# Optimization experiments

Measured on AMD Instinct MI355X. Metric: run time of the kernel, lower is better.

## Reference

```python
import jax, jax.numpy as jnp
import numpy as np
from jax import lax

T = 1.0      # terminal time
SIGMA = 1.0  # diffusion coefficient
N, D, P, M, H = 16384, 16, 8, 50, 128


def setup_inputs() -> dict:
    key = jax.random.key(0)
    ks = jax.random.split(key, 8)
    scale1 = 1.0 / np.sqrt(1 + D + P)
    scale2 = 1.0 / np.sqrt(H)
    return {
        "initial_states": jax.random.normal(ks[0], (N, D), jnp.float32),
        "initial_values": jax.random.normal(ks[1], (N,), jnp.float32),
        "observations": jax.random.normal(ks[2], (N, P), jnp.float32),
        "noise": jax.random.normal(ks[3], (M, N, D), jnp.float32),
        "W1": jax.random.normal(ks[4], (1 + D + P, H), jnp.float32) * scale1,
        "b1": jnp.zeros((H,), jnp.float32),
        "W2": jax.random.normal(ks[5], (H, H), jnp.float32) * scale2,
        "b2": jnp.zeros((H,), jnp.float32),
        "W3": jax.random.normal(ks[6], (H, D), jnp.float32) * scale2,
        "b3": jnp.zeros((D,), jnp.float32),
    }


def reference(initial_states, initial_values, observations, noise,
              W1, b1, W2, b2, W3, b3):
    """Euler-Maruyama rollout of simulate_SDEs: joint (X, V) SDE with
    per-step Z-network drift. drift b(X) = -X (OU process)."""
    m_steps = noise.shape[0]
    dt = jnp.asarray(T / m_steps, initial_states.dtype)
    sqrt_dt = jnp.sqrt(dt)
    times = jnp.arange(m_steps, dtype=initial_states.dtype) * dt  # time[m]

    def z_net(t, X, Y):
        tcol = jnp.full((X.shape[0], 1), t, X.dtype)
        h = jnp.concatenate([tcol, X, Y], axis=1)      # (N, 1+d+p)
        h = jax.nn.relu(h @ W1 + b1)
        h = jax.nn.relu(h @ W2 + b2)
        return h @ W3 + b3                             # (N, d)

    def step(carry, inp):
        X, V = carry
        eps, t = inp
        Wn = sqrt_dt * eps                             # Brownian increment
        Z = z_net(t, X, observations)
        drift_V = 0.5 * jnp.sum(Z * Z, axis=1)
        V = V + dt * drift_V + jnp.sum(Z * Wn, axis=1)
        X = X + dt * (-X) + SIGMA * Wn                 # b(X) = -X
        return (X, V), None

    (X, V), _ = lax.scan(step, (initial_states, initial_values), (noise, times))
    return X, V
```

## Files before the change

kernel.cpp:

```cpp
#include <hip/hip_runtime.h>

typedef __bf16   bf16x8 __attribute__((ext_vector_type(8)));
typedef float    f32x4  __attribute__((ext_vector_type(4)));
typedef float    f32x2  __attribute__((ext_vector_type(2)));
typedef uint32_t u32x4  __attribute__((ext_vector_type(4)));

constexpr int N_ = 16384;
constexpr int D_ = 16;
constexpr int P_ = 8;
constexpr int H_ = 128;
constexpr int M_ = 50;

__device__ __forceinline__ uint32_t pk_bf16(float a, float b) {
    uint32_t ua = __builtin_bit_cast(uint32_t, a) + 0x8000u;
    uint32_t ub = __builtin_bit_cast(uint32_t, b) + 0x8000u;
    return __builtin_amdgcn_perm(ub, ua, 0x07060302u);
}
__device__ __forceinline__ uint32_t cvtpk(float a, float b) {
    uint32_t r;
    asm("v_cvt_pk_bf16_f32 %0, %1, %2" : "=v"(r) : "v"(a), "v"(b));
    return r;
}
__device__ __forceinline__ uint32_t cvtpk_relu(float a, float b) {
    return cvtpk(fmaxf(a, 0.0f), fmaxf(b, 0.0f));
}

__device__ __forceinline__ bf16x8 lds_ldv(const bf16x8* p) {
    u32x4 v = *(volatile const u32x4*)p;
    return __builtin_bit_cast(bf16x8, v);
}

__global__ __launch_bounds__(128, 2)
void sde_fused(const float* __restrict__ X0,
               const float* __restrict__ V0,
               const float* __restrict__ Yobs,
               const float* __restrict__ noise,
               const float* __restrict__ W1, const float* __restrict__ b1,
               const float* __restrict__ W2, const float* __restrict__ b2,
               const float* __restrict__ W3, const float* __restrict__ b3,
               float* __restrict__ out)
{
    const int tid  = threadIdx.x;
    const int lane = tid & 63;
    const int half = tid >> 6;
    const int n    = lane & 15;
    const int q    = lane >> 4;
    const int gr   = blockIdx.x * 16 + n;

    const float dt   = 0.02f;
    const float sqdt = 0.1414213562373095f;

    __shared__ bf16x8 w2lds[8][4][64];
    __shared__ float  vpart[16];

#pragma unroll
    for (int cc = 0; cc < 4; ++cc) {
        const int ct = half * 4 + cc;
#pragma unroll
        for (int kt = 0; kt < 4; ++kt) {
            u32x4 u;
#pragma unroll
            for (int w = 0; w < 4; ++w) {
                int h0 = (kt * 2 + (w >> 1)) * 16 + q * 4 + (w & 1) * 2;
                u[w] = pk_bf16(W2[h0 * H_ + ct * 16 + n],
                               W2[(h0 + 1) * H_ + ct * 16 + n]);
            }
            w2lds[ct][kt][lane] = __builtin_bit_cast(bf16x8, u);
        }
    }

    bf16x8 w1f[8];
#pragma unroll
    for (int ct = 0; ct < 8; ++ct) {
        u32x4 u;
        u[0] = pk_bf16(W1[(1 + q * 4 + 0) * H_ + ct * 16 + n],
                       W1[(1 + q * 4 + 1) * H_ + ct * 16 + n]);
        u[1] = pk_bf16(W1[(1 + q * 4 + 2) * H_ + ct * 16 + n],
                       W1[(1 + q * 4 + 3) * H_ + ct * 16 + n]);
        u[2] = pk_bf16(W1[(17 + q * 2 + 0) * H_ + ct * 16 + n],
                       W1[(17 + q * 2 + 1) * H_ + ct * 16 + n]);
        u[3] = (q == 0) ? pk_bf16(b1[ct * 16 + n], W1[ct * 16 + n]) : 0u;
        w1f[ct] = __builtin_bit_cast(bf16x8, u);
    }
    bf16x8 w3f[4];
#pragma unroll
    for (int kt = 0; kt < 4; ++kt) {
        u32x4 u;
#pragma unroll
        for (int w = 0; w < 4; ++w) {
            int h0 = (kt * 2 + (w >> 1)) * 16 + q * 4 + (w & 1) * 2;
            u[w] = pk_bf16(W3[h0 * D_ + n], W3[(h0 + 1) * D_ + n]);
        }
        w3f[kt] = __builtin_bit_cast(bf16x8, u);
    }
    f32x4 b2r[8];
#pragma unroll
    for (int ct = 0; ct < 8; ++ct)
#pragma unroll
        for (int r = 0; r < 4; ++r) b2r[ct][r] = b2[ct * 16 + q * 4 + r];
    f32x4 b3r;
#pragma unroll
    for (int r = 0; r < 4; ++r) b3r[r] = b3[q * 4 + r];

    __syncthreads();

    f32x4 x = *(const f32x4*)&X0[gr * D_ + q * 4];
    f32x2 y2 = *(const f32x2*)&Yobs[gr * P_ + q * 2];
    const uint32_t yw = pk_bf16(y2[0], y2[1]);
    const float* npb = noise + (size_t)gr * D_ + q * 4;

    if (half == 1) {
#pragma unroll 2
        for (int m = 0; m < 25; ++m) {
            f32x4 e = *(const f32x4*)(npb + (size_t)m * N_ * D_);
#pragma unroll
            for (int r = 0; r < 4; ++r)
                x[r] = fmaf(x[r], 0.98f, sqdt * e[r]);
        }
    }

    const int s0 = half * 25;
    float t = half ? 0.5f : 0.0f;
    f32x4 e0 = *(const f32x4*)(npb + (size_t)s0 * N_ * D_);
    float vacc = 0.0f;

#pragma unroll 1
    for (int i = 0; i < 25; ++i) {
        const int m  = s0 + i;
        const int mn = (m + 1 < M_) ? (m + 1) : (M_ - 1);
        f32x4 e1 = *(const f32x4*)(npb + (size_t)mn * N_ * D_);

        u32x4 au;
        au[0] = cvtpk(x[0], x[1]);
        au[1] = cvtpk(x[2], x[3]);
        au[2] = yw;
        au[3] = (q == 0) ? cvtpk(1.0f, t) : 0u;
        bf16x8 a0 = __builtin_bit_cast(bf16x8, au);

        f32x4 h1c[8];
#pragma unroll
        for (int ct = 0; ct < 8; ++ct)
            h1c[ct] = __builtin_amdgcn_mfma_f32_16x16x32_bf16(
                w1f[ct], a0, (f32x4){0.f, 0.f, 0.f, 0.f}, 0, 0, 0);

        bf16x8 h1b[4];
#pragma unroll
        for (int kt = 0; kt < 4; ++kt) {
            u32x4 u;
            u[0] = cvtpk_relu(h1c[2 * kt][0], h1c[2 * kt][1]);
            u[1] = cvtpk_relu(h1c[2 * kt][2], h1c[2 * kt][3]);
            u[2] = cvtpk_relu(h1c[2 * kt + 1][0], h1c[2 * kt + 1][1]);
            u[3] = cvtpk_relu(h1c[2 * kt + 1][2], h1c[2 * kt + 1][3]);
            h1b[kt] = __builtin_bit_cast(bf16x8, u);
        }

        bf16x8 w2buf[2][4];
#pragma unroll
        for (int kt = 0; kt < 4; ++kt) w2buf[0][kt] = lds_ldv(&w2lds[0][kt][lane]);

        f32x4 hprev;
        bf16x8 h2b[4];
#pragma unroll
        for (int ct = 0; ct < 8; ++ct) {
            if (ct < 7) {
#pragma unroll
                for (int kt = 0; kt < 4; ++kt)
                    w2buf[(ct + 1) & 1][kt] = lds_ldv(&w2lds[ct + 1][kt][lane]);
            }
            f32x4 c = b2r[ct];
#pragma unroll
            for (int kt = 0; kt < 4; ++kt)
                c = __builtin_amdgcn_mfma_f32_16x16x32_bf16(
                    w2buf[ct & 1][kt], h1b[kt], c, 0, 0, 0);
            if ((ct & 1) == 0) {
                hprev = c;
            } else {
                u32x4 u;
                u[0] = cvtpk_relu(hprev[0], hprev[1]);
                u[1] = cvtpk_relu(hprev[2], hprev[3]);
                u[2] = cvtpk_relu(c[0], c[1]);
                u[3] = cvtpk_relu(c[2], c[3]);
                h2b[ct >> 1] = __builtin_bit_cast(bf16x8, u);
            }
        }

        f32x4 za = __builtin_amdgcn_mfma_f32_16x16x32_bf16(w3f[0], h2b[0], b3r, 0, 0, 0);
        za = __builtin_amdgcn_mfma_f32_16x16x32_bf16(w3f[1], h2b[1], za, 0, 0, 0);
        f32x4 zb = __builtin_amdgcn_mfma_f32_16x16x32_bf16(
            w3f[2], h2b[2], (f32x4){0.f, 0.f, 0.f, 0.f}, 0, 0, 0);
        zb = __builtin_amdgcn_mfma_f32_16x16x32_bf16(w3f[3], h2b[3], zb, 0, 0, 0);

#pragma unroll
        for (int r = 0; r < 4; ++r) {
            float z  = za[r] + zb[r];
            float wn = sqdt * e0[r];
            vacc = fmaf(z, wn, fmaf(0.01f * z, z, vacc));
            x[r] = fmaf(x[r], 0.98f, wn);
        }

        e0 = e1;
        t += dt;
    }

    float part = vacc;
    part += __shfl_xor(part, 16);
    part += __shfl_xor(part, 32);

    if (half == 0 && q == 0) vpart[n] = part;
    __syncthreads();
    if (half == 1) {
        *(f32x4*)&out[gr * D_ + q * 4] = x;
        if (q == 0) out[N_ * D_ + gr] = V0[gr] + vpart[n] + part;
    }
}

extern "C" void kernel_launch(void* const* d_in, const int* in_sizes, int n_in,
                              void* d_out, int out_size, void* d_ws, size_t ws_size,
                              hipStream_t stream)
{
    const float* X0 = (const float*)d_in[0];
    const float* V0 = (const float*)d_in[1];
    const float* Y  = (const float*)d_in[2];
    const float* nz = (const float*)d_in[3];
    const float* W1 = (const float*)d_in[4];
    const float* b1 = (const float*)d_in[5];
    const float* W2 = (const float*)d_in[6];
    const float* b2 = (const float*)d_in[7];
    const float* W3 = (const float*)d_in[8];
    const float* b3 = (const float*)d_in[9];
    float* out = (float*)d_out;

    sde_fused<<<N_ / 16, 128, 0, stream>>>(X0, V0, Y, nz, W1, b1, W2, b2, W3, b3, out);
}
```

Baseline: 158.7 us.

## Keep W2 in registers and stream W1, W3 and b2 from LDS

Swaps which weights live where. W2 fragments (32 bf16x8) are now held in VGPRs instead of being reloaded from LDS every step. The smaller W1, W3 and b2 operands move to a shared LDS buffer and are software-prefetched around the MFMA chains. The layer-1 MFMAs and ReLU packing are also interleaved with the W1 prefetches. This aims to cut per-step LDS traffic and latency on the largest GEMM, at the cost of higher register pressure under launch_bounds(128,2) and extra LDS loads for the smaller matrices.

```diff
diff --git a/kernel.cpp b/kernel.cpp
--- a/kernel.cpp
+++ b/kernel.cpp
@@ -25,9 +25,13 @@
     return cvtpk(fmaxf(a, 0.0f), fmaxf(b, 0.0f));
 }
 
-__device__ __forceinline__ bf16x8 lds_ldv(const bf16x8* p) {
+__device__ __forceinline__ bf16x8 lds_ldv8(const void* p) {
     u32x4 v = *(volatile const u32x4*)p;
     return __builtin_bit_cast(bf16x8, v);
+}
+__device__ __forceinline__ f32x4 lds_ldvf(const void* p) {
+    u32x4 v = *(volatile const u32x4*)p;
+    return __builtin_bit_cast(f32x4, v);
 }
 
 __global__ __launch_bounds__(128, 2)
@@ -50,12 +54,39 @@
     const float dt   = 0.02f;
     const float sqdt = 0.1414213562373095f;
 
-    __shared__ bf16x8 w2lds[8][4][64];
-    __shared__ float  vpart[16];
-
-#pragma unroll
-    for (int cc = 0; cc < 4; ++cc) {
-        const int ct = half * 4 + cc;
+    __shared__ __align__(16) unsigned char smem[12864];
+
+    if (half == 0) {
+#pragma unroll
+        for (int ct = 0; ct < 8; ++ct) {
+            u32x4 u;
+            u[0] = pk_bf16(W1[(1 + q * 4 + 0) * H_ + ct * 16 + n],
+                           W1[(1 + q * 4 + 1) * H_ + ct * 16 + n]);
+            u[1] = pk_bf16(W1[(1 + q * 4 + 2) * H_ + ct * 16 + n],
+                           W1[(1 + q * 4 + 3) * H_ + ct * 16 + n]);
+            u[2] = pk_bf16(W1[(17 + q * 2 + 0) * H_ + ct * 16 + n],
+                           W1[(17 + q * 2 + 1) * H_ + ct * 16 + n]);
+            u[3] = (q == 0) ? pk_bf16(b1[ct * 16 + n], W1[ct * 16 + n]) : 0u;
+            *(u32x4*)(smem + ct * 1024 + lane * 16) = u;
+            __builtin_amdgcn_sched_barrier(0);
+        }
+#pragma unroll
+        for (int kt = 0; kt < 4; ++kt) {
+            u32x4 u;
+#pragma unroll
+            for (int w = 0; w < 4; ++w) {
+                int h0 = (kt * 2 + (w >> 1)) * 16 + q * 4 + (w & 1) * 2;
+                u[w] = pk_bf16(W3[h0 * D_ + n], W3[(h0 + 1) * D_ + n]);
+            }
+            *(u32x4*)(smem + 8192 + kt * 1024 + lane * 16) = u;
+            __builtin_amdgcn_sched_barrier(0);
+        }
+        if (lane < 32) *(f32x4*)(smem + 12288 + lane * 16) = *(const f32x4*)&b2[lane * 4];
+    }
+
+    bf16x8 w2f[8][4];
+#pragma unroll
+    for (int ct = 0; ct < 8; ++ct) {
 #pragma unroll
         for (int kt = 0; kt < 4; ++kt) {
             u32x4 u;
@@ -65,42 +96,12 @@
                 u[w] = pk_bf16(W2[h0 * H_ + ct * 16 + n],
                                W2[(h0 + 1) * H_ + ct * 16 + n]);
             }
-            w2lds[ct][kt][lane] = __builtin_bit_cast(bf16x8, u);
-        }
-    }
-
-    bf16x8 w1f[8];
-#pragma unroll
-    for (int ct = 0; ct < 8; ++ct) {
-        u32x4 u;
-        u[0] = pk_bf16(W1[(1 + q * 4 + 0) * H_ + ct * 16 + n],
-                       W1[(1 + q * 4 + 1) * H_ + ct * 16 + n]);
-        u[1] = pk_bf16(W1[(1 + q * 4 + 2) * H_ + ct * 16 + n],
-                       W1[(1 + q * 4 + 3) * H_ + ct * 16 + n]);
-        u[2] = pk_bf16(W1[(17 + q * 2 + 0) * H_ + ct * 16 + n],
-                       W1[(17 + q * 2 + 1) * H_ + ct * 16 + n]);
-        u[3] = (q == 0) ? pk_bf16(b1[ct * 16 + n], W1[ct * 16 + n]) : 0u;
-        w1f[ct] = __builtin_bit_cast(bf16x8, u);
-    }
-    bf16x8 w3f[4];
-#pragma unroll
-    for (int kt = 0; kt < 4; ++kt) {
-        u32x4 u;
-#pragma unroll
-        for (int w = 0; w < 4; ++w) {
-            int h0 = (kt * 2 + (w >> 1)) * 16 + q * 4 + (w & 1) * 2;
-            u[w] = pk_bf16(W3[h0 * D_ + n], W3[(h0 + 1) * D_ + n]);
-        }
-        w3f[kt] = __builtin_bit_cast(bf16x8, u);
-    }
-    f32x4 b2r[8];
-#pragma unroll
-    for (int ct = 0; ct < 8; ++ct)
-#pragma unroll
-        for (int r = 0; r < 4; ++r) b2r[ct][r] = b2[ct * 16 + q * 4 + r];
-    f32x4 b3r;
-#pragma unroll
-    for (int r = 0; r < 4; ++r) b3r[r] = b3[q * 4 + r];
+            w2f[ct][kt] = __builtin_bit_cast(bf16x8, u);
+        }
+        __builtin_amdgcn_sched_barrier(0);
+    }
+
+    f32x4 b3r = *(const f32x4*)&b3[q * 4];
 
     __syncthreads();
 
@@ -123,6 +124,19 @@
     float t = half ? 0.5f : 0.0f;
     f32x4 e0 = *(const f32x4*)(npb + (size_t)s0 * N_ * D_);
     float vacc = 0.0f;
+
+    const uint32_t lofs = (uint32_t)lane * 16u;
+    const uint32_t qofs = (uint32_t)q * 16u;
+
+    bf16x8 w1buf[4];
+#pragma unroll
+    for (int k = 0; k < 4; ++k) w1buf[k] = lds_ldv8(smem + k * 1024 + lofs);
+    bf16x8 w3buf[2];
+    w3buf[0] = lds_ldv8(smem + 8192 + 0 * 1024 + lofs);
+    w3buf[1] = lds_ldv8(smem + 8192 + 1 * 1024 + lofs);
+    f32x4 b2buf[2];
+    b2buf[0] = lds_ldvf(smem + 12288 + 0 * 64 + qofs);
+    b2buf[1] = lds_ldvf(smem + 12288 + 1 * 64 + qofs);
 
 #pragma unroll 1
     for (int i = 0; i < 25; ++i) {
@@ -137,58 +151,58 @@
         au[3] = (q == 0) ? cvtpk(1.0f, t) : 0u;
         bf16x8 a0 = __builtin_bit_cast(bf16x8, au);
 
-        f32x4 h1c[8];
-#pragma unroll
-        for (int ct = 0; ct < 8; ++ct)
-            h1c[ct] = __builtin_amdgcn_mfma_f32_16x16x32_bf16(
-                w1f[ct], a0, (f32x4){0.f, 0.f, 0.f, 0.f}, 0, 0, 0);
-
         bf16x8 h1b[4];
-#pragma unroll
-        for (int kt = 0; kt < 4; ++kt) {
-            u32x4 u;
-            u[0] = cvtpk_relu(h1c[2 * kt][0], h1c[2 * kt][1]);
-            u[1] = cvtpk_relu(h1c[2 * kt][2], h1c[2 * kt][3]);
-            u[2] = cvtpk_relu(h1c[2 * kt + 1][0], h1c[2 * kt + 1][1]);
-            u[3] = cvtpk_relu(h1c[2 * kt + 1][2], h1c[2 * kt + 1][3]);
-            h1b[kt] = __builtin_bit_cast(bf16x8, u);
-        }
-
-        bf16x8 w2buf[2][4];
-#pragma unroll
-        for (int kt = 0; kt < 4; ++kt) w2buf[0][kt] = lds_ldv(&w2lds[0][kt][lane]);
-
-        f32x4 hprev;
-        bf16x8 h2b[4];
+        f32x4 hodd;
 #pragma unroll
         for (int ct = 0; ct < 8; ++ct) {
-            if (ct < 7) {
-#pragma unroll
-                for (int kt = 0; kt < 4; ++kt)
-                    w2buf[(ct + 1) & 1][kt] = lds_ldv(&w2lds[ct + 1][kt][lane]);
-            }
-            f32x4 c = b2r[ct];
-#pragma unroll
-            for (int kt = 0; kt < 4; ++kt)
-                c = __builtin_amdgcn_mfma_f32_16x16x32_bf16(
-                    w2buf[ct & 1][kt], h1b[kt], c, 0, 0, 0);
+            const int b = ct & 3;
+            f32x4 h = __builtin_amdgcn_mfma_f32_16x16x32_bf16(
+                w1buf[b], a0, (f32x4){0.f, 0.f, 0.f, 0.f}, 0, 0, 0);
+            w1buf[b] = lds_ldv8(smem + ((ct + 4) & 7) * 1024 + lofs);
             if ((ct & 1) == 0) {
-                hprev = c;
+                hodd = h;
             } else {
                 u32x4 u;
-                u[0] = cvtpk_relu(hprev[0], hprev[1]);
-                u[1] = cvtpk_relu(hprev[2], hprev[3]);
-                u[2] = cvtpk_relu(c[0], c[1]);
-                u[3] = cvtpk_relu(c[2], c[3]);
-                h2b[ct >> 1] = __builtin_bit_cast(bf16x8, u);
+                u[0] = cvtpk_relu(hodd[0], hodd[1]);
+                u[1] = cvtpk_relu(hodd[2], hodd[3]);
+                u[2] = cvtpk_relu(h[0], h[1]);
+                u[3] = cvtpk_relu(h[2], h[3]);
+                h1b[ct >> 1] = __builtin_bit_cast(bf16x8, u);
             }
         }
 
-        f32x4 za = __builtin_amdgcn_mfma_f32_16x16x32_bf16(w3f[0], h2b[0], b3r, 0, 0, 0);
-        za = __builtin_amdgcn_mfma_f32_16x16x32_bf16(w3f[1], h2b[1], za, 0, 0, 0);
+        bf16x8 h2b[4];
+#pragma unroll
+        for (int ctp = 0; ctp < 4; ++ctp) {
+            f32x4 c0 = b2buf[0];
+            f32x4 c1 = b2buf[1];
+            b2buf[0] = lds_ldvf(smem + 12288 + ((2 * ctp + 2) & 7) * 64 + qofs);
+            b2buf[1] = lds_ldvf(smem + 12288 + ((2 * ctp + 3) & 7) * 64 + qofs);
+#pragma unroll
+            for (int kt = 0; kt < 4; ++kt)
+                c0 = __builtin_amdgcn_mfma_f32_16x16x32_bf16(
+                    w2f[2 * ctp][kt], h1b[kt], c0, 0, 0, 0);
+#pragma unroll
+            for (int kt = 0; kt < 4; ++kt)
+                c1 = __builtin_amdgcn_mfma_f32_16x16x32_bf16(
+                    w2f[2 * ctp + 1][kt], h1b[kt], c1, 0, 0, 0);
+            u32x4 u;
+            u[0] = cvtpk_relu(c0[0], c0[1]);
+            u[1] = cvtpk_relu(c0[2], c0[3]);
+            u[2] = cvtpk_relu(c1[0], c1[1]);
+            u[3] = cvtpk_relu(c1[2], c1[3]);
+            h2b[ctp] = __builtin_bit_cast(bf16x8, u);
+        }
+
+        f32x4 za = __builtin_amdgcn_mfma_f32_16x16x32_bf16(w3buf[0], h2b[0], b3r, 0, 0, 0);
+        w3buf[0] = lds_ldv8(smem + 8192 + 2 * 1024 + lofs);
+        za = __builtin_amdgcn_mfma_f32_16x16x32_bf16(w3buf[1], h2b[1], za, 0, 0, 0);
+        w3buf[1] = lds_ldv8(smem + 8192 + 3 * 1024 + lofs);
         f32x4 zb = __builtin_amdgcn_mfma_f32_16x16x32_bf16(
-            w3f[2], h2b[2], (f32x4){0.f, 0.f, 0.f, 0.f}, 0, 0, 0);
-        zb = __builtin_amdgcn_mfma_f32_16x16x32_bf16(w3f[3], h2b[3], zb, 0, 0, 0);
+            w3buf[0], h2b[2], (f32x4){0.f, 0.f, 0.f, 0.f}, 0, 0, 0);
+        w3buf[0] = lds_ldv8(smem + 8192 + 0 * 1024 + lofs);
+        zb = __builtin_amdgcn_mfma_f32_16x16x32_bf16(w3buf[1], h2b[3], zb, 0, 0, 0);
+        w3buf[1] = lds_ldv8(smem + 8192 + 1 * 1024 + lofs);
 
 #pragma unroll
         for (int r = 0; r < 4; ++r) {
@@ -206,11 +220,12 @@
     part += __shfl_xor(part, 16);
     part += __shfl_xor(part, 32);
 
-    if (half == 0 && q == 0) vpart[n] = part;
+    if (half == 0 && q == 0) *(float*)(smem + 12800 + n * 4) = part;
     __syncthreads();
     if (half == 1) {
         *(f32x4*)&out[gr * D_ + q * 4] = x;
-        if (q == 0) out[N_ * D_ + gr] = V0[gr] + vpart[n] + part;
+        if (q == 0)
+            out[N_ * D_ + gr] = V0[gr] + *(const float*)(smem + 12800 + n * 4) + part;
     }
 }
 
```

Result: slower. 172.3 us (+8.5%).

## Switch MLP to 32x32x16 MFMA with register-resident W2, 32 rows per block

Applied to the files above, without the earlier changes.

Replaces the 16x16x32 MFMA tiling with 32x32x16 MFMAs, so each block handles 32 samples instead of 16. All of W2 is now held in registers (4x8 bf16x8 fragments per lane) instead of being staged through LDS and reloaded every step, and the b2 bias is injected through an extra rank-1 MFMA. The goal is to cut LDS traffic and per-sample instruction overhead. In exchange register pressure rises sharply, so launch bounds drop to one block per SIMD-equivalent, the grid halves to 512 blocks and occupancy falls, which may leave latency exposed. The W3 MFMA also wastes half its output rows because D is 16.

```diff
diff --git a/kernel.cpp b/kernel.cpp
--- a/kernel.cpp
+++ b/kernel.cpp
@@ -2,7 +2,7 @@
 
 typedef __bf16   bf16x8 __attribute__((ext_vector_type(8)));
 typedef float    f32x4  __attribute__((ext_vector_type(4)));
-typedef float    f32x2  __attribute__((ext_vector_type(2)));
+typedef float    f32x16 __attribute__((ext_vector_type(16)));
 typedef uint32_t u32x4  __attribute__((ext_vector_type(4)));
 
 constexpr int N_ = 16384;
@@ -25,12 +25,7 @@
     return cvtpk(fmaxf(a, 0.0f), fmaxf(b, 0.0f));
 }
 
-__device__ __forceinline__ bf16x8 lds_ldv(const bf16x8* p) {
-    u32x4 v = *(volatile const u32x4*)p;
-    return __builtin_bit_cast(bf16x8, v);
-}
-
-__global__ __launch_bounds__(128, 2)
+__global__ __launch_bounds__(128, 1)
 void sde_fused(const float* __restrict__ X0,
                const float* __restrict__ V0,
                const float* __restrict__ Yobs,
@@ -43,174 +38,214 @@
     const int tid  = threadIdx.x;
     const int lane = tid & 63;
     const int half = tid >> 6;
-    const int n    = lane & 15;
-    const int q    = lane >> 4;
-    const int gr   = blockIdx.x * 16 + n;
+    const int n    = lane & 31;
+    const int hi   = lane >> 5;
+    const int gr   = blockIdx.x * 32 + n;
 
     const float dt   = 0.02f;
     const float sqdt = 0.1414213562373095f;
 
-    __shared__ bf16x8 w2lds[8][4][64];
-    __shared__ float  vpart[16];
-
-#pragma unroll
-    for (int cc = 0; cc < 4; ++cc) {
-        const int ct = half * 4 + cc;
-#pragma unroll
-        for (int kt = 0; kt < 4; ++kt) {
+    const f32x16 Z16 = {0.f,0.f,0.f,0.f,0.f,0.f,0.f,0.f,
+                        0.f,0.f,0.f,0.f,0.f,0.f,0.f,0.f};
+
+    bf16x8 a1f[4][2];
+#pragma unroll
+    for (int mt = 0; mt < 4; ++mt) {
+        const int col = mt * 32 + n;
+        u32x4 u;
+        u[0] = pk_bf16(W1[(1 + 4*hi) * H_ + col],  W1[(2 + 4*hi) * H_ + col]);
+        u[1] = pk_bf16(W1[(3 + 4*hi) * H_ + col],  W1[(4 + 4*hi) * H_ + col]);
+        u[2] = pk_bf16(W1[(9 + 4*hi) * H_ + col],  W1[(10 + 4*hi) * H_ + col]);
+        u[3] = pk_bf16(W1[(11 + 4*hi) * H_ + col], W1[(12 + 4*hi) * H_ + col]);
+        a1f[mt][0] = __builtin_bit_cast(bf16x8, u);
+        u32x4 v;
+        v[0] = hi ? pk_bf16(W1[0 * H_ + col], b1[col])
+                  : pk_bf16(W1[17 * H_ + col], W1[18 * H_ + col]);
+        v[1] = hi ? 0u : pk_bf16(W1[19 * H_ + col], W1[20 * H_ + col]);
+        v[2] = hi ? 0u : pk_bf16(W1[21 * H_ + col], W1[22 * H_ + col]);
+        v[3] = hi ? 0u : pk_bf16(W1[23 * H_ + col], W1[24 * H_ + col]);
+        a1f[mt][1] = __builtin_bit_cast(bf16x8, v);
+    }
+
+    bf16x8 a2f[4][8], a2b[4];
+#pragma unroll
+    for (int mt = 0; mt < 4; ++mt) {
+        const int col = mt * 32 + n;
+#pragma unroll
+        for (int kt = 0; kt < 8; ++kt) {
+            const int r0 = kt * 16 + 4 * hi;
             u32x4 u;
-#pragma unroll
-            for (int w = 0; w < 4; ++w) {
-                int h0 = (kt * 2 + (w >> 1)) * 16 + q * 4 + (w & 1) * 2;
-                u[w] = pk_bf16(W2[h0 * H_ + ct * 16 + n],
-                               W2[(h0 + 1) * H_ + ct * 16 + n]);
-            }
-            w2lds[ct][kt][lane] = __builtin_bit_cast(bf16x8, u);
-        }
-    }
-
-    bf16x8 w1f[8];
-#pragma unroll
-    for (int ct = 0; ct < 8; ++ct) {
+            u[0] = pk_bf16(W2[(r0 + 0) * H_ + col],  W2[(r0 + 1) * H_ + col]);
+            u[1] = pk_bf16(W2[(r0 + 2) * H_ + col],  W2[(r0 + 3) * H_ + col]);
+            u[2] = pk_bf16(W2[(r0 + 8) * H_ + col],  W2[(r0 + 9) * H_ + col]);
+            u[3] = pk_bf16(W2[(r0 + 10) * H_ + col], W2[(r0 + 11) * H_ + col]);
+            a2f[mt][kt] = __builtin_bit_cast(bf16x8, u);
+        }
+        u32x4 ub;
+        ub[0] = hi ? 0u : pk_bf16(b2[col], 0.0f);
+        ub[1] = 0u; ub[2] = 0u; ub[3] = 0u;
+        a2b[mt] = __builtin_bit_cast(bf16x8, ub);
+    }
+
+    bf16x8 a3f[8];
+    const bool mv = (n < 16);
+#pragma unroll
+    for (int kt = 0; kt < 8; ++kt) {
+        const int r0 = kt * 16 + 4 * hi;
+        float f0 = mv ? W3[(r0 + 0) * D_ + n] : 0.0f;
+        float f1 = mv ? W3[(r0 + 1) * D_ + n] : 0.0f;
+        float f2 = mv ? W3[(r0 + 2) * D_ + n] : 0.0f;
+        float f3 = mv ? W3[(r0 + 3) * D_ + n] : 0.0f;
+        float f4 = mv ? W3[(r0 + 8) * D_ + n] : 0.0f;
+        float f5 = mv ? W3[(r0 + 9) * D_ + n] : 0.0f;
+        float f6 = mv ? W3[(r0 + 10) * D_ + n] : 0.0f;
+        float f7 = mv ? W3[(r0 + 11) * D_ + n] : 0.0f;
         u32x4 u;
-        u[0] = pk_bf16(W1[(1 + q * 4 + 0) * H_ + ct * 16 + n],
-                       W1[(1 + q * 4 + 1) * H_ + ct * 16 + n]);
-        u[1] = pk_bf16(W1[(1 + q * 4 + 2) * H_ + ct * 16 + n],
-                       W1[(1 + q * 4 + 3) * H_ + ct * 16 + n]);
-        u[2] = pk_bf16(W1[(17 + q * 2 + 0) * H_ + ct * 16 + n],
-                       W1[(17 + q * 2 + 1) * H_ + ct * 16 + n]);
-        u[3] = (q == 0) ? pk_bf16(b1[ct * 16 + n], W1[ct * 16 + n]) : 0u;
-        w1f[ct] = __builtin_bit_cast(bf16x8, u);
-    }
-    bf16x8 w3f[4];
-#pragma unroll
-    for (int kt = 0; kt < 4; ++kt) {
-        u32x4 u;
-#pragma unroll
-        for (int w = 0; w < 4; ++w) {
-            int h0 = (kt * 2 + (w >> 1)) * 16 + q * 4 + (w & 1) * 2;
-            u[w] = pk_bf16(W3[h0 * D_ + n], W3[(h0 + 1) * D_ + n]);
-        }
-        w3f[kt] = __builtin_bit_cast(bf16x8, u);
-    }
-    f32x4 b2r[8];
-#pragma unroll
-    for (int ct = 0; ct < 8; ++ct)
-#pragma unroll
-        for (int r = 0; r < 4; ++r) b2r[ct][r] = b2[ct * 16 + q * 4 + r];
-    f32x4 b3r;
-#pragma unroll
-    for (int r = 0; r < 4; ++r) b3r[r] = b3[q * 4 + r];
-
-    __syncthreads();
-
-    f32x4 x = *(const f32x4*)&X0[gr * D_ + q * 4];
-    f32x2 y2 = *(const f32x2*)&Yobs[gr * P_ + q * 2];
-    const uint32_t yw = pk_bf16(y2[0], y2[1]);
-    const float* npb = noise + (size_t)gr * D_ + q * 4;
+        u[0] = pk_bf16(f0, f1);
+        u[1] = pk_bf16(f2, f3);
+        u[2] = pk_bf16(f4, f5);
+        u[3] = pk_bf16(f6, f7);
+        a3f[kt] = __builtin_bit_cast(bf16x8, u);
+    }
+
+    f32x16 b3c = Z16;
+#pragma unroll
+    for (int r = 0; r < 8; ++r) b3c[r] = b3[(r & 3) + 8 * (r >> 2) + 4 * hi];
+
+    u32x4 fbu;
+    fbu[0] = hi ? 0u : pk_bf16(1.0f, 0.0f);
+    fbu[1] = 0u; fbu[2] = 0u; fbu[3] = 0u;
+    const bf16x8 fbias = __builtin_bit_cast(bf16x8, fbu);
+
+    f32x4 y0 = *(const f32x4*)&Yobs[gr * P_];
+    f32x4 y1 = *(const f32x4*)&Yobs[gr * P_ + 4];
+    const uint32_t yw0 = pk_bf16(y0[0], y0[1]);
+    const uint32_t yw1 = pk_bf16(y0[2], y0[3]);
+    const uint32_t yw2 = pk_bf16(y1[0], y1[1]);
+    const uint32_t yw3 = pk_bf16(y1[2], y1[3]);
+
+    f32x4 xA = *(const f32x4*)&X0[gr * D_ + 4 * hi];
+    f32x4 xB = *(const f32x4*)&X0[gr * D_ + 8 + 4 * hi];
+    const float* npb = noise + (size_t)gr * D_ + 4 * hi;
 
     if (half == 1) {
 #pragma unroll 2
         for (int m = 0; m < 25; ++m) {
-            f32x4 e = *(const f32x4*)(npb + (size_t)m * N_ * D_);
-#pragma unroll
-            for (int r = 0; r < 4; ++r)
-                x[r] = fmaf(x[r], 0.98f, sqdt * e[r]);
+            f32x4 eA = *(const f32x4*)(npb + (size_t)m * N_ * D_);
+            f32x4 eB = *(const f32x4*)(npb + (size_t)m * N_ * D_ + 8);
+#pragma unroll
+            for (int r = 0; r < 4; ++r) {
+                xA[r] = fmaf(xA[r], 0.98f, sqdt * eA[r]);
+                xB[r] = fmaf(xB[r], 0.98f, sqdt * eB[r]);
+            }
         }
     }
 
     const int s0 = half * 25;
     float t = half ? 0.5f : 0.0f;
-    f32x4 e0 = *(const f32x4*)(npb + (size_t)s0 * N_ * D_);
+    f32x4 eA0 = *(const f32x4*)(npb + (size_t)s0 * N_ * D_);
+    f32x4 eB0 = *(const f32x4*)(npb + (size_t)s0 * N_ * D_ + 8);
     float vacc = 0.0f;
 
 #pragma unroll 1
     for (int i = 0; i < 25; ++i) {
         const int m  = s0 + i;
         const int mn = (m + 1 < M_) ? (m + 1) : (M_ - 1);
-        f32x4 e1 = *(const f32x4*)(npb + (size_t)mn * N_ * D_);
-
-        u32x4 au;
-        au[0] = cvtpk(x[0], x[1]);
-        au[1] = cvtpk(x[2], x[3]);
-        au[2] = yw;
-        au[3] = (q == 0) ? cvtpk(1.0f, t) : 0u;
-        bf16x8 a0 = __builtin_bit_cast(bf16x8, au);
-
-        f32x4 h1c[8];
-#pragma unroll
-        for (int ct = 0; ct < 8; ++ct)
-            h1c[ct] = __builtin_amdgcn_mfma_f32_16x16x32_bf16(
-                w1f[ct], a0, (f32x4){0.f, 0.f, 0.f, 0.f}, 0, 0, 0);
-
-        bf16x8 h1b[4];
-#pragma unroll
-        for (int kt = 0; kt < 4; ++kt) {
+        f32x4 eA1 = *(const f32x4*)(npb + (size_t)mn * N_ * D_);
+        f32x4 eB1 = *(const f32x4*)(npb + (size_t)mn * N_ * D_ + 8);
+
+        u32x4 g0u;
+        g0u[0] = cvtpk(xA[0], xA[1]);
+        g0u[1] = cvtpk(xA[2], xA[3]);
+        g0u[2] = cvtpk(xB[0], xB[1]);
+        g0u[3] = cvtpk(xB[2], xB[3]);
+        bf16x8 g0 = __builtin_bit_cast(bf16x8, g0u);
+        u32x4 g1u;
+        g1u[0] = hi ? cvtpk(t, 1.0f) : yw0;
+        g1u[1] = hi ? 0u : yw1;
+        g1u[2] = hi ? 0u : yw2;
+        g1u[3] = hi ? 0u : yw3;
+        bf16x8 g1 = __builtin_bit_cast(bf16x8, g1u);
+
+        f32x16 acc1[4];
+#pragma unroll
+        for (int mt = 0; mt < 4; ++mt) {
+            f32x16 c = __builtin_amdgcn_mfma_f32_32x32x16_bf16(a1f[mt][0], g0, Z16, 0, 0, 0);
+            acc1[mt]  = __builtin_amdgcn_mfma_f32_32x32x16_bf16(a1f[mt][1], g1, c, 0, 0, 0);
+        }
+
+        bf16x8 hb[8];
+#pragma unroll
+        for (int kt = 0; kt < 8; ++kt) {
+            const int r0 = 8 * (kt & 1);
+            const f32x16 A = acc1[kt >> 1];
             u32x4 u;
-            u[0] = cvtpk_relu(h1c[2 * kt][0], h1c[2 * kt][1]);
-            u[1] = cvtpk_relu(h1c[2 * kt][2], h1c[2 * kt][3]);
-            u[2] = cvtpk_relu(h1c[2 * kt + 1][0], h1c[2 * kt + 1][1]);
-            u[3] = cvtpk_relu(h1c[2 * kt + 1][2], h1c[2 * kt + 1][3]);
-            h1b[kt] = __builtin_bit_cast(bf16x8, u);
-        }
-
-        bf16x8 w2buf[2][4];
-#pragma unroll
-        for (int kt = 0; kt < 4; ++kt) w2buf[0][kt] = lds_ldv(&w2lds[0][kt][lane]);
-
-        f32x4 hprev;
-        bf16x8 h2b[4];
-#pragma unroll
-        for (int ct = 0; ct < 8; ++ct) {
-            if (ct < 7) {
-#pragma unroll
-                for (int kt = 0; kt < 4; ++kt)
-                    w2buf[(ct + 1) & 1][kt] = lds_ldv(&w2lds[ct + 1][kt][lane]);
-            }
-            f32x4 c = b2r[ct];
-#pragma unroll
-            for (int kt = 0; kt < 4; ++kt)
-                c = __builtin_amdgcn_mfma_f32_16x16x32_bf16(
-                    w2buf[ct & 1][kt], h1b[kt], c, 0, 0, 0);
-            if ((ct & 1) == 0) {
-                hprev = c;
-            } else {
-                u32x4 u;
-                u[0] = cvtpk_relu(hprev[0], hprev[1]);
-                u[1] = cvtpk_relu(hprev[2], hprev[3]);
-                u[2] = cvtpk_relu(c[0], c[1]);
-                u[3] = cvtpk_relu(c[2], c[3]);
-                h2b[ct >> 1] = __builtin_bit_cast(bf16x8, u);
-            }
-        }
-
-        f32x4 za = __builtin_amdgcn_mfma_f32_16x16x32_bf16(w3f[0], h2b[0], b3r, 0, 0, 0);
-        za = __builtin_amdgcn_mfma_f32_16x16x32_bf16(w3f[1], h2b[1], za, 0, 0, 0);
-        f32x4 zb = __builtin_amdgcn_mfma_f32_16x16x32_bf16(
-            w3f[2], h2b[2], (f32x4){0.f, 0.f, 0.f, 0.f}, 0, 0, 0);
-        zb = __builtin_amdgcn_mfma_f32_16x16x32_bf16(w3f[3], h2b[3], zb, 0, 0, 0);
+            u[0] = cvtpk_relu(A[r0 + 0], A[r0 + 1]);
+            u[1] = cvtpk_relu(A[r0 + 2], A[r0 + 3]);
+            u[2] = cvtpk_relu(A[r0 + 4], A[r0 + 5]);
+            u[3] = cvtpk_relu(A[r0 + 6], A[r0 + 7]);
+            hb[kt] = __builtin_bit_cast(bf16x8, u);
+        }
+
+        f32x16 acc2[4];
+#pragma unroll
+        for (int mt = 0; mt < 4; ++mt) {
+            f32x16 c = __builtin_amdgcn_mfma_f32_32x32x16_bf16(a2b[mt], fbias, Z16, 0, 0, 0);
+#pragma unroll
+            for (int kt = 0; kt < 8; ++kt)
+                c = __builtin_amdgcn_mfma_f32_32x32x16_bf16(a2f[mt][kt], hb[kt], c, 0, 0, 0);
+            acc2[mt] = c;
+        }
+
+        bf16x8 gb[8];
+#pragma unroll
+        for (int kt = 0; kt < 8; ++kt) {
+            const int r0 = 8 * (kt & 1);
+            const f32x16 A = acc2[kt >> 1];
+            u32x4 u;
+            u[0] = cvtpk_relu(A[r0 + 0], A[r0 + 1]);
+            u[1] = cvtpk_relu(A[r0 + 2], A[r0 + 3]);
+            u[2] = cvtpk_relu(A[r0 + 4], A[r0 + 5]);
+            u[3] = cvtpk_relu(A[r0 + 6], A[r0 + 7]);
+            gb[kt] = __builtin_bit_cast(bf16x8, u);
+        }
+
+        f32x16 acc3 = b3c;
+#pragma unroll
+        for (int kt = 0; kt < 8; ++kt)
+            acc3 = __builtin_amdgcn_mfma_f32_32x32x16_bf16(a3f[kt], gb[kt], acc3, 0, 0, 0);
 
 #pragma unroll
         for (int r = 0; r < 4; ++r) {
-            float z  = za[r] + zb[r];
-            float wn = sqdt * e0[r];
+            float z  = acc3[r];
+            float wn = sqdt * eA0[r];
             vacc = fmaf(z, wn, fmaf(0.01f * z, z, vacc));
-            x[r] = fmaf(x[r], 0.98f, wn);
-        }
-
-        e0 = e1;
+        }
+#pragma unroll
+        for (int r = 0; r < 4; ++r) {
+            float z  = acc3[4 + r];
+            float wn = sqdt * eB0[r];
+            vacc = fmaf(z, wn, fmaf(0.01f * z, z, vacc));
+        }
+#pragma unroll
+        for (int r = 0; r < 4; ++r) {
+            xA[r] = fmaf(xA[r], 0.98f, sqdt * eA0[r]);
+            xB[r] = fmaf(xB[r], 0.98f, sqdt * eB0[r]);
+        }
+
+        eA0 = eA1; eB0 = eB1;
         t += dt;
     }
 
-    float part = vacc;
-    part += __shfl_xor(part, 16);
-    part += __shfl_xor(part, 32);
-
-    if (half == 0 && q == 0) vpart[n] = part;
+    vacc += __shfl_xor(vacc, 32);
+
+    __shared__ float vsh[32];
+    if (half == 0 && hi == 0) vsh[n] = vacc;
     __syncthreads();
     if (half == 1) {
-        *(f32x4*)&out[gr * D_ + q * 4] = x;
-        if (q == 0) out[N_ * D_ + gr] = V0[gr] + vpart[n] + part;
+        *(f32x4*)&out[gr * D_ + 4 * hi] = xA;
+        *(f32x4*)&out[gr * D_ + 8 + 4 * hi] = xB;
+        if (hi == 0) out[N_ * D_ + gr] = V0[gr] + vsh[n] + vacc;
     }
 }
 
@@ -230,5 +265,5 @@
     const float* b3 = (const float*)d_in[9];
     float* out = (float*)d_out;
 
-    sde_fused<<<N_ / 16, 128, 0, stream>>>(X0, V0, Y, nz, W1, b1, W2, b2, W3, b3, out);
-}
+    sde_fused<<<N_ / 32, 128, 0, stream>>>(X0, V0, Y, nz, W1, b1, W2, b2, W3, b3, out);
+}
```

Measured after the change: 156.2 us. Within noise of the previous version (-1.6%).
